# Kernel tuning notes

Hardware: AMD Instinct MI355X
Metric: run time of the kernel (lower is better)

The kernel has to match this reference:

```python
import jax, jax.numpy as jnp
import numpy as np

B, N, D, E = 2, 512, 128, 64
H, HS, FF = 8, 16, 512
EPS = 1e-6

def _glorot(key, shape, fan_in, fan_out):
    limit = np.sqrt(6.0 / (fan_in + fan_out))
    return jax.random.uniform(key, shape, jnp.float32, -limit, limit)

def setup_inputs() -> dict:
    key = jax.random.key(0)
    ks = jax.random.split(key, 12)
    node = jax.random.normal(ks[0], (B, N, D), jnp.float32)
    edge = jax.random.normal(ks[1], (B, N, N, E), jnp.float32)
    Wq = _glorot(ks[2], (H, D, HS), D, HS)
    Wk = _glorot(ks[3], (H, D + E, HS), D + E, HS)
    Wv = _glorot(ks[4], (H, D, HS), D, HS)
    Wp = _glorot(ks[5], (H, HS, D), H * HS, D)
    bp = jnp.zeros((D,), jnp.float32)
    ln1_g = jnp.ones((D,), jnp.float32)
    ln1_b = jnp.zeros((D,), jnp.float32)
    Wf1 = _glorot(ks[6], (D, FF), D, FF)
    bf1 = jnp.zeros((FF,), jnp.float32)
    Wf2 = _glorot(ks[7], (FF, D), FF, D)
    bf2 = jnp.zeros((D,), jnp.float32)
    ln2_g = jnp.ones((D,), jnp.float32)
    ln2_b = jnp.zeros((D,), jnp.float32)
    return dict(node=node, edge=edge, Wq=Wq, Wk=Wk, Wv=Wv, Wp=Wp, bp=bp,
                ln1_g=ln1_g, ln1_b=ln1_b, Wf1=Wf1, bf1=bf1, Wf2=Wf2, bf2=bf2,
                ln2_g=ln2_g, ln2_b=ln2_b)

def _layernorm(x, g, b):
    mu = jnp.mean(x, axis=-1, keepdims=True)
    var = jnp.mean(jnp.square(x - mu), axis=-1, keepdims=True)
    return (x - mu) * jax.lax.rsqrt(var + EPS) * g + b

def reference(node, edge, Wq, Wk, Wv, Wp, bp, ln1_g, ln1_b, Wf1, bf1, Wf2, bf2, ln2_g, ln2_b):
    # --- edge-conditioned multi-head attention ---
    # query scaled by sqrt(head_size), as in the TF code
    q = jnp.einsum('bni,hio->bnho', node, Wq) / jnp.sqrt(jnp.asarray(HS, node.dtype))
    # concat([repeat(key), edge]) @ Wk  ==  key @ Wk[:, :D]  +  edge @ Wk[:, D:]
    Wk_node, Wk_edge = Wk[:, :D, :], Wk[:, D:, :]
    k_node = jnp.einsum('bmi,hio->bmho', node, Wk_node)           # [B,M,H,HS]
    logits_node = jnp.einsum('bnho,bmho->bhnm', q, k_node)        # [B,H,N,M]
    # contract q with edge-kernel first (small), then with edge (memory-bound pass)
    qe = jnp.einsum('bnho,heo->bnhe', q, Wk_edge)                 # [B,N,H,E]
    logits_edge = jnp.einsum('bnme,bnhe->bhnm', edge, qe)         # [B,H,N,M]
    attn = jax.nn.softmax(logits_node + logits_edge, axis=-1)
    v = jnp.einsum('bmi,hio->bmho', node, Wv)                     # [B,M,H,HS]
    mh = jnp.einsum('bhnm,bmho->bnho', attn, v)                   # [B,N,H,HS]
    attn_out = jnp.einsum('bnho,hoi->bni', mh, Wp) + bp           # [B,N,D]
    # --- residual + layernorm ---
    x = _layernorm(node + attn_out, ln1_g, ln1_b)
    # --- FFN: relu dense -> dense, residual + layernorm ---
    ff = jnp.maximum(x @ Wf1 + bf1, 0.0) @ Wf2 + bf2
    return _layernorm(x + ff, ln2_g, ln2_b)
```

## Files before the change

### kernel.cpp

```cpp
#include <hip/hip_runtime.h>
#include <cstdint>
#include <cmath>

#define BB 2
#define NN 512
#define DD 128
#define EE 64
#define HH 8
#define HSS 16
#define FFF 512
#define EPSF 1e-6f

__global__ __launch_bounds__(256)
void qkv_kernel(const float* __restrict__ node,
                const float* __restrict__ Wq,
                const float* __restrict__ Wk,
                const float* __restrict__ Wv,
                float* __restrict__ q_g,
                float* __restrict__ k_t,
                float* __restrict__ v_t,
                float* __restrict__ qe_g) {
  int r0 = blockIdx.x * 4;
  int t = threadIdx.x;
  int b = r0 >> 9;
  int n0 = r0 & 511;
  __shared__ float nrow[4][DD];
  __shared__ float qrow[4][DD];

  nrow[t >> 7][t & 127] = node[(size_t)r0*DD + t];
  {
    int idx = t + 256;
    nrow[idx >> 7][idx & 127] = node[(size_t)r0*DD + idx];
  }
  __syncthreads();

  if (t < 128) {
    int h = t >> 4, o = t & 15;
    float aq[4] = {0.f,0.f,0.f,0.f}, av[4] = {0.f,0.f,0.f,0.f};
    const float* wq = Wq + h*(DD*HSS) + o;
    const float* wv = Wv + h*(DD*HSS) + o;
    for (int i = 0; i < DD; ++i) {
      float wqi = wq[i*HSS], wvi = wv[i*HSS];
      #pragma unroll
      for (int r = 0; r < 4; ++r) {
        float x = nrow[r][i];
        aq[r] += x * wqi;
        av[r] += x * wvi;
      }
    }
    #pragma unroll
    for (int r = 0; r < 4; ++r) {
      float qq = aq[r] * 0.25f;
      q_g[(size_t)(r0+r)*128 + t] = qq;
      qrow[r][t] = qq;
    }
    float* vtp = v_t + ((size_t)(b*HH + h)*HSS + o)*NN + n0;
    *(float4*)vtp = make_float4(av[0], av[1], av[2], av[3]);
  } else {
    int tt = t - 128, h = tt >> 4, o = tt & 15;
    float ak[4] = {0.f,0.f,0.f,0.f};
    const float* wk = Wk + h*((DD+EE)*HSS) + o;
    for (int i = 0; i < DD; ++i) {
      float wki = wk[i*HSS];
      #pragma unroll
      for (int r = 0; r < 4; ++r) ak[r] += nrow[r][i] * wki;
    }
    float* ktp = k_t + ((size_t)(b*HH + h)*HSS + o)*NN + n0;
    *(float4*)ktp = make_float4(ak[0], ak[1], ak[2], ak[3]);
  }
  __syncthreads();

  for (int idx = t; idx < HH*EE; idx += 256) {
    int h = idx >> 6, e = idx & 63;
    const float* wke = Wk + (h*(DD+EE) + DD + e)*HSS;
    float w[HSS];
    #pragma unroll
    for (int o = 0; o < HSS; ++o) w[o] = wke[o];
    #pragma unroll
    for (int r = 0; r < 4; ++r) {
      float a = 0.f;
      #pragma unroll
      for (int o = 0; o < HSS; ++o) a += qrow[r][h*HSS + o] * w[o];
      qe_g[(size_t)(r0+r)*(HH*EE) + idx] = a;
    }
  }
}

__global__ __launch_bounds__(256)
void attn_kernel(const float* __restrict__ node,
                 const float* __restrict__ edge,
                 const float* __restrict__ q_g,
                 const float* __restrict__ k_t,
                 const float* __restrict__ v_t,
                 const float* __restrict__ qe_g,
                 const float* __restrict__ Wp,
                 const float* __restrict__ bp,
                 const float* __restrict__ ln1_g,
                 const float* __restrict__ ln1_b,
                 float* __restrict__ x_g) {
  int bn = blockIdx.x;
  int b = bn >> 9;
  int t = threadIdx.x;
  int h = t >> 5, ml = t & 31;
  __shared__ float4 et[2][32][16];
  __shared__ float mh_s[HH*HSS];
  __shared__ float red[4];

  float4 qe_r[16];
  const float4* qep = (const float4*)(qe_g + (size_t)bn*(HH*EE) + h*EE);
  #pragma unroll
  for (int j = 0; j < 16; ++j) qe_r[j] = qep[j];
  float q_r[16];
  const float* qp = q_g + (size_t)bn*128 + h*HSS;
  #pragma unroll
  for (int o = 0; o < 16; ++o) q_r[o] = qp[o];

  const float4* e_base = (const float4*)(edge + (size_t)bn*NN*EE);
  const float* kt_base = k_t + (size_t)(b*HH + h)*HSS*NN;
  const float* vt_base = v_t + (size_t)(b*HH + h)*HSS*NN;

  int ra = t >> 4,        ja = t & 15;         int ca = (ja + ra) & 15;
  int rb = (t + 256) >> 4, jb = t & 15;        int cb = (jb + rb) & 15;

  float4 f0 = e_base[(size_t)(ra)*16 + ja];
  float4 f1 = e_base[(size_t)(rb)*16 + jb];

  float lg[16];
  for (int c = 0; c < 16; ++c) {
    int buf = c & 1;
    et[buf][ra][ca] = f0;
    et[buf][rb][cb] = f1;
    __syncthreads();
    if (c < 15) {
      f0 = e_base[(size_t)((c+1)*32 + ra)*16 + ja];
      f1 = e_base[(size_t)((c+1)*32 + rb)*16 + jb];
    }
    int m = c*32 + ml;
    float acc = 0.f;
    #pragma unroll
    for (int j = 0; j < 16; ++j) {
      float4 e4 = et[buf][ml][(j + ml) & 15];
      acc += e4.x*qe_r[j].x + e4.y*qe_r[j].y + e4.z*qe_r[j].z + e4.w*qe_r[j].w;
    }
    const float* kp = kt_base + m;
    #pragma unroll
    for (int o = 0; o < 16; ++o) acc += q_r[o] * kp[o*NN];
    lg[c] = acc;
  }

  float mx = lg[0];
  #pragma unroll
  for (int c = 1; c < 16; ++c) mx = fmaxf(mx, lg[c]);
  #pragma unroll
  for (int off = 1; off < 32; off <<= 1) mx = fmaxf(mx, __shfl_xor(mx, off, 64));
  float sum = 0.f;
  #pragma unroll
  for (int c = 0; c < 16; ++c) { lg[c] = __expf(lg[c] - mx); sum += lg[c]; }
  #pragma unroll
  for (int off = 1; off < 32; off <<= 1) sum += __shfl_xor(sum, off, 64);
  float inv = 1.f / sum;

  float mh_acc[16];
  #pragma unroll
  for (int z = 0; z < 16; ++z) mh_acc[z] = 0.f;
  for (int c = 0; c < 16; ++c) {
    float p = lg[c] * inv;
    const float* vp = vt_base + c*32 + ml;
    #pragma unroll
    for (int o = 0; o < 16; ++o) mh_acc[o] += p * vp[o*NN];
  }
  #pragma unroll
  for (int z = 0; z < 16; ++z) {
    #pragma unroll
    for (int off = 1; off < 32; off <<= 1)
      mh_acc[z] += __shfl_xor(mh_acc[z], off, 64);
  }
  if (ml == 0) {
    #pragma unroll
    for (int z = 0; z < 16; ++z) mh_s[h*16 + z] = mh_acc[z];
  }
  __syncthreads();

  float val = 0.f;
  if (t < 128) {
    float a = bp[t];
    #pragma unroll 4
    for (int ho = 0; ho < 128; ++ho) a += mh_s[ho] * Wp[ho*128 + t];
    val = node[(size_t)bn*128 + t] + a;
    float s1 = val, s2 = val*val;
    #pragma unroll
    for (int off = 1; off < 64; off <<= 1) {
      s1 += __shfl_xor(s1, off, 64);
      s2 += __shfl_xor(s2, off, 64);
    }
    if ((t & 63) == 0) { red[(t>>6)*2] = s1; red[(t>>6)*2 + 1] = s2; }
  }
  __syncthreads();
  if (t < 128) {
    float s1 = red[0] + red[2], s2 = red[1] + red[3];
    float mu = s1 * (1.f/128.f);
    float var = s2 * (1.f/128.f) - mu*mu;
    float xh = (val - mu) * rsqrtf(var + EPSF);
    x_g[(size_t)bn*128 + t] = xh * ln1_g[t] + ln1_b[t];
  }
}

__global__ __launch_bounds__(256)
void ffn_kernel(const float* __restrict__ x_g,
                const float* __restrict__ Wf1,
                const float* __restrict__ bf1,
                const float* __restrict__ Wf2,
                const float* __restrict__ bf2,
                const float* __restrict__ ln2_g,
                const float* __restrict__ ln2_b,
                float* __restrict__ out) {
  int t = threadIdx.x;
  int row0 = blockIdx.x * 8;
  __shared__ float xs[8][128];
  __shared__ float hs[8][FFF];
  __shared__ float red2[4][4][2];

  #pragma unroll
  for (int k = 0; k < 4; ++k) {
    int idx = t + k*256;
    ((float*)xs)[idx] = x_g[(size_t)row0*128 + idx];
  }
  __syncthreads();

  float acc[8][2];
  #pragma unroll
  for (int r = 0; r < 8; ++r) { acc[r][0] = bf1[t]; acc[r][1] = bf1[t + 256]; }
  for (int i = 0; i < 128; ++i) {
    float w0 = Wf1[i*512 + t];
    float w1 = Wf1[i*512 + t + 256];
    #pragma unroll
    for (int r = 0; r < 8; ++r) {
      float xv = xs[r][i];
      acc[r][0] += xv * w0;
      acc[r][1] += xv * w1;
    }
  }
  #pragma unroll
  for (int r = 0; r < 8; ++r) {
    hs[r][t]       = fmaxf(acc[r][0], 0.f);
    hs[r][t + 256] = fmaxf(acc[r][1], 0.f);
  }
  __syncthreads();

  int i = t & 127, rg = t >> 7;
  float o_[4];
  #pragma unroll
  for (int r = 0; r < 4; ++r) o_[r] = bf2[i];
  for (int j = 0; j < 512; ++j) {
    float w = Wf2[j*128 + i];
    #pragma unroll
    for (int r = 0; r < 4; ++r) o_[r] += hs[rg*4 + r][j] * w;
  }

  int w_ = t >> 6;
  float va[4], s1[4], s2[4];
  #pragma unroll
  for (int r = 0; r < 4; ++r) {
    va[r] = o_[r] + xs[rg*4 + r][i];
    s1[r] = va[r]; s2[r] = va[r]*va[r];
  }
  #pragma unroll
  for (int off = 1; off < 64; off <<= 1) {
    #pragma unroll
    for (int r = 0; r < 4; ++r) {
      s1[r] += __shfl_xor(s1[r], off, 64);
      s2[r] += __shfl_xor(s2[r], off, 64);
    }
  }
  if ((t & 63) == 0) {
    #pragma unroll
    for (int r = 0; r < 4; ++r) { red2[w_][r][0] = s1[r]; red2[w_][r][1] = s2[r]; }
  }
  __syncthreads();
  int pw = w_ ^ 1;
  #pragma unroll
  for (int r = 0; r < 4; ++r) {
    float S1 = red2[w_][r][0] + red2[pw][r][0];
    float S2 = red2[w_][r][1] + red2[pw][r][1];
    float mu = S1 * (1.f/128.f);
    float var = S2 * (1.f/128.f) - mu*mu;
    out[((size_t)row0 + rg*4 + r)*128 + i] =
        (va[r] - mu) * rsqrtf(var + EPSF) * ln2_g[i] + ln2_b[i];
  }
}

extern "C" void kernel_launch(void* const* d_in, const int* in_sizes, int n_in,
                              void* d_out, int out_size, void* d_ws, size_t ws_size,
                              hipStream_t stream) {
  const float* node  = (const float*)d_in[0];
  const float* edge  = (const float*)d_in[1];
  const float* Wq    = (const float*)d_in[2];
  const float* Wk    = (const float*)d_in[3];
  const float* Wv    = (const float*)d_in[4];
  const float* Wp    = (const float*)d_in[5];
  const float* bp    = (const float*)d_in[6];
  const float* ln1_g = (const float*)d_in[7];
  const float* ln1_b = (const float*)d_in[8];
  const float* Wf1   = (const float*)d_in[9];
  const float* bf1   = (const float*)d_in[10];
  const float* Wf2   = (const float*)d_in[11];
  const float* bf2   = (const float*)d_in[12];
  const float* ln2_g = (const float*)d_in[13];
  const float* ln2_b = (const float*)d_in[14];
  float* out = (float*)d_out;

  float* ws   = (float*)d_ws;
  float* q_g  = ws;
  float* qe_g = ws + 131072;
  float* k_t  = ws + 655360;
  float* v_t  = ws + 786432;
  float* x_g  = ws + 917504;

  qkv_kernel<<<(BB*NN)/4, 256, 0, stream>>>(node, Wq, Wk, Wv, q_g, k_t, v_t, qe_g);
  attn_kernel<<<BB*NN, 256, 0, stream>>>(node, edge, q_g, k_t, v_t, qe_g,
                                         Wp, bp, ln1_g, ln1_b, x_g);
  ffn_kernel<<<(BB*NN)/8, 256, 0, stream>>>(x_g, Wf1, bf1, Wf2, bf2,
                                            ln2_g, ln2_b, out);
}
```

Before: 370.2 us.

## Increase parallelism in QKV, attention, and FFN kernels by shrinking per-block work

The QKV kernel now processes 2 rows per block instead of 4. The attention kernel uses 512 threads, so each head gets a full 64-lane wavefront, and it stages 64 edge rows per iteration in 8 chunks instead of 16. The FFN kernel handles 2 rows per block and splits the second GEMM's reduction over FF across two thread halves, combining them through shared memory. The goal is more blocks and waves in flight, to hide latency on a kernel that is far from bandwidth-bound. The cost is more redundant weight reads per row and extra synchronisation.

Result: faster. 325.4 us (-12.1%).

```diff
diff --git a/kernel.cpp b/kernel.cpp
--- a/kernel.cpp
+++ b/kernel.cpp
@@ -20,53 +20,48 @@
                 float* __restrict__ k_t,
                 float* __restrict__ v_t,
                 float* __restrict__ qe_g) {
-  int r0 = blockIdx.x * 4;
+  int r0 = blockIdx.x * 2;
   int t = threadIdx.x;
   int b = r0 >> 9;
   int n0 = r0 & 511;
-  __shared__ float nrow[4][DD];
-  __shared__ float qrow[4][DD];
+  __shared__ float nrow[2][DD];
+  __shared__ float qrow[2][DD];
 
   nrow[t >> 7][t & 127] = node[(size_t)r0*DD + t];
-  {
-    int idx = t + 256;
-    nrow[idx >> 7][idx & 127] = node[(size_t)r0*DD + idx];
-  }
   __syncthreads();
 
   if (t < 128) {
     int h = t >> 4, o = t & 15;
-    float aq[4] = {0.f,0.f,0.f,0.f}, av[4] = {0.f,0.f,0.f,0.f};
+    float aq[2] = {0.f,0.f}, av[2] = {0.f,0.f};
     const float* wq = Wq + h*(DD*HSS) + o;
     const float* wv = Wv + h*(DD*HSS) + o;
     for (int i = 0; i < DD; ++i) {
       float wqi = wq[i*HSS], wvi = wv[i*HSS];
       #pragma unroll
-      for (int r = 0; r < 4; ++r) {
+      for (int r = 0; r < 2; ++r) {
         float x = nrow[r][i];
         aq[r] += x * wqi;
         av[r] += x * wvi;
       }
     }
     #pragma unroll
-    for (int r = 0; r < 4; ++r) {
+    for (int r = 0; r < 2; ++r) {
       float qq = aq[r] * 0.25f;
       q_g[(size_t)(r0+r)*128 + t] = qq;
       qrow[r][t] = qq;
     }
-    float* vtp = v_t + ((size_t)(b*HH + h)*HSS + o)*NN + n0;
-    *(float4*)vtp = make_float4(av[0], av[1], av[2], av[3]);
+    *(float2*)(v_t + ((size_t)(b*HH + (t>>4))*HSS + (t&15))*NN + n0) =
+        make_float2(av[0], av[1]);
   } else {
     int tt = t - 128, h = tt >> 4, o = tt & 15;
-    float ak[4] = {0.f,0.f,0.f,0.f};
+    float ak[2] = {0.f,0.f};
     const float* wk = Wk + h*((DD+EE)*HSS) + o;
     for (int i = 0; i < DD; ++i) {
       float wki = wk[i*HSS];
       #pragma unroll
-      for (int r = 0; r < 4; ++r) ak[r] += nrow[r][i] * wki;
-    }
-    float* ktp = k_t + ((size_t)(b*HH + h)*HSS + o)*NN + n0;
-    *(float4*)ktp = make_float4(ak[0], ak[1], ak[2], ak[3]);
+      for (int r = 0; r < 2; ++r) ak[r] += nrow[r][i] * wki;
+    }
+    *(float2*)(k_t + ((size_t)(b*HH + h)*HSS + o)*NN + n0) = make_float2(ak[0], ak[1]);
   }
   __syncthreads();
 
@@ -75,18 +70,18 @@
     const float* wke = Wk + (h*(DD+EE) + DD + e)*HSS;
     float w[HSS];
     #pragma unroll
-    for (int o = 0; o < HSS; ++o) w[o] = wke[o];
-    #pragma unroll
-    for (int r = 0; r < 4; ++r) {
+    for (int o = 0; o < 16; ++o) w[o] = wke[o];
+    #pragma unroll
+    for (int r = 0; r < 2; ++r) {
       float a = 0.f;
       #pragma unroll
-      for (int o = 0; o < HSS; ++o) a += qrow[r][h*HSS + o] * w[o];
+      for (int o = 0; o < 16; ++o) a += qrow[r][h*HSS + o] * w[o];
       qe_g[(size_t)(r0+r)*(HH*EE) + idx] = a;
     }
   }
 }
 
-__global__ __launch_bounds__(256)
+__global__ __launch_bounds__(512)
 void attn_kernel(const float* __restrict__ node,
                  const float* __restrict__ edge,
                  const float* __restrict__ q_g,
@@ -101,8 +96,8 @@
   int bn = blockIdx.x;
   int b = bn >> 9;
   int t = threadIdx.x;
-  int h = t >> 5, ml = t & 31;
-  __shared__ float4 et[2][32][16];
+  int h = t >> 6, ml = t & 63;
+  __shared__ float4 et[2][64][16];
   __shared__ float mh_s[HH*HSS];
   __shared__ float red[4];
 
@@ -119,23 +114,23 @@
   const float* kt_base = k_t + (size_t)(b*HH + h)*HSS*NN;
   const float* vt_base = v_t + (size_t)(b*HH + h)*HSS*NN;
 
-  int ra = t >> 4,        ja = t & 15;         int ca = (ja + ra) & 15;
-  int rb = (t + 256) >> 4, jb = t & 15;        int cb = (jb + rb) & 15;
-
-  float4 f0 = e_base[(size_t)(ra)*16 + ja];
-  float4 f1 = e_base[(size_t)(rb)*16 + jb];
-
-  float lg[16];
-  for (int c = 0; c < 16; ++c) {
+  int ra = t >> 4,          ja = t & 15;   int ca = (ja + ra) & 15;
+  int rb = (t + 512) >> 4,  jb = t & 15;   int cb = (jb + rb) & 15;
+
+  float4 f0 = e_base[(size_t)ra*16 + ja];
+  float4 f1 = e_base[(size_t)rb*16 + jb];
+
+  float lg[8];
+  for (int c = 0; c < 8; ++c) {
     int buf = c & 1;
     et[buf][ra][ca] = f0;
     et[buf][rb][cb] = f1;
     __syncthreads();
-    if (c < 15) {
-      f0 = e_base[(size_t)((c+1)*32 + ra)*16 + ja];
-      f1 = e_base[(size_t)((c+1)*32 + rb)*16 + jb];
-    }
-    int m = c*32 + ml;
+    if (c < 7) {
+      f0 = e_base[(size_t)((c+1)*64 + ra)*16 + ja];
+      f1 = e_base[(size_t)((c+1)*64 + rb)*16 + jb];
+    }
+    int m = c*64 + ml;
     float acc = 0.f;
     #pragma unroll
     for (int j = 0; j < 16; ++j) {
@@ -150,29 +145,29 @@
 
   float mx = lg[0];
   #pragma unroll
-  for (int c = 1; c < 16; ++c) mx = fmaxf(mx, lg[c]);
-  #pragma unroll
-  for (int off = 1; off < 32; off <<= 1) mx = fmaxf(mx, __shfl_xor(mx, off, 64));
+  for (int c = 1; c < 8; ++c) mx = fmaxf(mx, lg[c]);
+  #pragma unroll
+  for (int off = 1; off < 64; off <<= 1) mx = fmaxf(mx, __shfl_xor(mx, off, 64));
   float sum = 0.f;
   #pragma unroll
-  for (int c = 0; c < 16; ++c) { lg[c] = __expf(lg[c] - mx); sum += lg[c]; }
-  #pragma unroll
-  for (int off = 1; off < 32; off <<= 1) sum += __shfl_xor(sum, off, 64);
+  for (int c = 0; c < 8; ++c) { lg[c] = __expf(lg[c] - mx); sum += lg[c]; }
+  #pragma unroll
+  for (int off = 1; off < 64; off <<= 1) sum += __shfl_xor(sum, off, 64);
   float inv = 1.f / sum;
 
   float mh_acc[16];
   #pragma unroll
   for (int z = 0; z < 16; ++z) mh_acc[z] = 0.f;
-  for (int c = 0; c < 16; ++c) {
+  for (int c = 0; c < 8; ++c) {
     float p = lg[c] * inv;
-    const float* vp = vt_base + c*32 + ml;
+    const float* vp = vt_base + c*64 + ml;
     #pragma unroll
     for (int o = 0; o < 16; ++o) mh_acc[o] += p * vp[o*NN];
   }
   #pragma unroll
   for (int z = 0; z < 16; ++z) {
     #pragma unroll
-    for (int off = 1; off < 32; off <<= 1)
+    for (int off = 1; off < 64; off <<= 1)
       mh_acc[z] += __shfl_xor(mh_acc[z], off, 64);
   }
   if (ml == 0) {
@@ -215,78 +210,60 @@
                 const float* __restrict__ ln2_b,
                 float* __restrict__ out) {
   int t = threadIdx.x;
-  int row0 = blockIdx.x * 8;
-  __shared__ float xs[8][128];
-  __shared__ float hs[8][FFF];
-  __shared__ float red2[4][4][2];
-
-  #pragma unroll
-  for (int k = 0; k < 4; ++k) {
-    int idx = t + k*256;
-    ((float*)xs)[idx] = x_g[(size_t)row0*128 + idx];
-  }
-  __syncthreads();
-
-  float acc[8][2];
-  #pragma unroll
-  for (int r = 0; r < 8; ++r) { acc[r][0] = bf1[t]; acc[r][1] = bf1[t + 256]; }
+  int row0 = blockIdx.x * 2;
+  __shared__ float xs[2][128];
+  __shared__ float hs[2][FFF];
+  __shared__ float ps[2][2][128];
+  __shared__ float red2[4][2];
+
+  ((float*)xs)[t] = x_g[(size_t)row0*128 + t];
+  __syncthreads();
+
+  float a00 = bf1[t], a01 = bf1[t + 256];
+  float a10 = a00, a11 = a01;
   for (int i = 0; i < 128; ++i) {
     float w0 = Wf1[i*512 + t];
     float w1 = Wf1[i*512 + t + 256];
-    #pragma unroll
-    for (int r = 0; r < 8; ++r) {
-      float xv = xs[r][i];
-      acc[r][0] += xv * w0;
-      acc[r][1] += xv * w1;
-    }
-  }
-  #pragma unroll
-  for (int r = 0; r < 8; ++r) {
-    hs[r][t]       = fmaxf(acc[r][0], 0.f);
-    hs[r][t + 256] = fmaxf(acc[r][1], 0.f);
-  }
-  __syncthreads();
-
-  int i = t & 127, rg = t >> 7;
-  float o_[4];
-  #pragma unroll
-  for (int r = 0; r < 4; ++r) o_[r] = bf2[i];
-  for (int j = 0; j < 512; ++j) {
+    float x0 = xs[0][i], x1 = xs[1][i];
+    a00 += x0 * w0; a01 += x0 * w1;
+    a10 += x1 * w0; a11 += x1 * w1;
+  }
+  hs[0][t]       = fmaxf(a00, 0.f);
+  hs[0][t + 256] = fmaxf(a01, 0.f);
+  hs[1][t]       = fmaxf(a10, 0.f);
+  hs[1][t + 256] = fmaxf(a11, 0.f);
+  __syncthreads();
+
+  int i = t & 127, half = t >> 7;
+  float p0 = 0.f, p1 = 0.f;
+  for (int j = half*256; j < half*256 + 256; ++j) {
     float w = Wf2[j*128 + i];
-    #pragma unroll
-    for (int r = 0; r < 4; ++r) o_[r] += hs[rg*4 + r][j] * w;
-  }
+    p0 += hs[0][j] * w;
+    p1 += hs[1][j] * w;
+  }
+  ps[half][0][i] = p0;
+  ps[half][1][i] = p1;
+  __syncthreads();
+
+  int rg = half;
+  float va = bf2[i] + ps[0][rg][i] + ps[1][rg][i] + xs[rg][i];
 
   int w_ = t >> 6;
-  float va[4], s1[4], s2[4];
-  #pragma unroll
-  for (int r = 0; r < 4; ++r) {
-    va[r] = o_[r] + xs[rg*4 + r][i];
-    s1[r] = va[r]; s2[r] = va[r]*va[r];
-  }
+  float s1 = va, s2 = va*va;
   #pragma unroll
   for (int off = 1; off < 64; off <<= 1) {
-    #pragma unroll
-    for (int r = 0; r < 4; ++r) {
-      s1[r] += __shfl_xor(s1[r], off, 64);
-      s2[r] += __shfl_xor(s2[r], off, 64);
-    }
-  }
-  if ((t & 63) == 0) {
-    #pragma unroll
-    for (int r = 0; r < 4; ++r) { red2[w_][r][0] = s1[r]; red2[w_][r][1] = s2[r]; }
-  }
+    s1 += __shfl_xor(s1, off, 64);
+    s2 += __shfl_xor(s2, off, 64);
+  }
+  if ((t & 63) == 0) { red2[w_][0] = s1; red2[w_][1] = s2; }
   __syncthreads();
   int pw = w_ ^ 1;
-  #pragma unroll
-  for (int r = 0; r < 4; ++r) {
-    float S1 = red2[w_][r][0] + red2[pw][r][0];
-    float S2 = red2[w_][r][1] + red2[pw][r][1];
-    float mu = S1 * (1.f/128.f);
-    float var = S2 * (1.f/128.f) - mu*mu;
-    out[((size_t)row0 + rg*4 + r)*128 + i] =
-        (va[r] - mu) * rsqrtf(var + EPSF) * ln2_g[i] + ln2_b[i];
-  }
+  float S1 = red2[w_][0] + red2[pw][0];
+  float S2 = red2[w_][1] + red2[pw][1];
+  float mu = S1 * (1.f/128.f);
+  float var = S2 * (1.f/128.f) - mu*mu;
+  out[((size_t)row0 + rg)*128 + i] =
+      (va - mu) * rsqrtf(var + EPSF) * ln2_g[i] + ln2_b[i];
 }
 
 extern "C" void kernel_launch(void* const* d_in, const int* in_sizes, int n_in,
@@ -316,9 +293,9 @@
   float* v_t  = ws + 786432;
   float* x_g  = ws + 917504;
 
-  qkv_kernel<<<(BB*NN)/4, 256, 0, stream>>>(node, Wq, Wk, Wv, q_g, k_t, v_t, qe_g);
-  attn_kernel<<<BB*NN, 256, 0, stream>>>(node, edge, q_g, k_t, v_t, qe_g,
+  qkv_kernel<<<(BB*NN)/2, 256, 0, stream>>>(node, Wq, Wk, Wv, q_g, k_t, v_t, qe_g);
+  attn_kernel<<<BB*NN, 512, 0, stream>>>(node, edge, q_g, k_t, v_t, qe_g,
                                          Wp, bp, ln1_g, ln1_b, x_g);
-  ffn_kernel<<<(BB*NN)/8, 256, 0, stream>>>(x_g, Wf1, bf1, Wf2, bf2,
+  ffn_kernel<<<(BB*NN)/2, 256, 0, stream>>>(x_g, Wf1, bf1, Wf2, bf2,
                                             ln2_g, ln2_b, out);
 }
```
